# Kernel tuning notes

Measured on AMD Instinct MI355X. Metric: run time of the kernel, lower is better.

## Reference

```python
import jax, jax.numpy as jnp
import numpy as np

NUM_BINS = 256
SCALAR = 1.0


def _per_batch_hist(img):
    # img: [B, C, H, W] in [0,1]. torch.histc(img[i]*255, bins=256, min=0, max=255)
    # bin width = 255/256; value v maps to bin floor(v * 256/255), last edge -> bin 255.
    B = img.shape[0]
    x = img.reshape(B, -1) * 255.0
    idx = jnp.clip(jnp.floor(x * (NUM_BINS / 255.0)), 0, NUM_BINS - 1).astype(jnp.int32)
    # offset bin ids per batch item so one segment_sum builds all histograms
    seg = idx + (jnp.arange(B, dtype=jnp.int32)[:, None] * NUM_BINS)
    ones = jnp.ones_like(x)
    hist = jax.ops.segment_sum(ones.ravel(), seg.ravel(), num_segments=B * NUM_BINS)
    hist = hist.reshape(B, NUM_BINS)
    hist = hist / jnp.sum(hist, axis=1, keepdims=True)
    return hist.T  # [NUM_BINS, B] matching torch.stack(hist, dim=1)


def setup_inputs() -> dict:
    key = jax.random.key(0)
    k1, k2 = jax.random.split(key)
    im1 = jax.random.uniform(k1, (16, 3, 512, 512), dtype=jnp.float32)
    im2 = jax.random.uniform(k2, (16, 3, 512, 512), dtype=jnp.float32)
    return {"im1": im1, "im2": im2}


def reference(im1, im2):
    h1 = _per_batch_hist(im1)  # [256, B]
    h2 = _per_batch_hist(im2)
    c1 = jnp.cumsum(h1, axis=0)
    c2 = jnp.cumsum(h2, axis=0)
    emd = jnp.sum(jnp.abs(c1 - c2), axis=0)  # L1 over bin dim -> [B]
    total = jnp.sum(emd) / h2.shape[0] * SCALAR / 3.0
    return total
```

## Files before the change

### kernel.cpp

```cpp
#include <hip/hip_runtime.h>

#define NUM_BINS 256
#define PER_HIST 786432
#define BATCH 16
#define NHIST 32
#define CHUNKS 64
#define THREADS 256
#define ELEMS_PER_BLOCK (PER_HIST / CHUNKS)
#define VEC_PER_BLOCK (ELEMS_PER_BLOCK / 4)
#define ITERS (VEC_PER_BLOCK / THREADS)

typedef float floatx4 __attribute__((ext_vector_type(4)));

__global__ void zero_ws_kernel(unsigned int* __restrict__ ws) {
    ws[blockIdx.x * blockDim.x + threadIdx.x] = 0u;
}

__global__ __launch_bounds__(THREADS) void hist_kernel(const float* __restrict__ im1,
                                                       const float* __restrict__ im2,
                                                       unsigned int* __restrict__ hist) {
    __shared__ unsigned int lh[4][NUM_BINS];
    const int t = threadIdx.x;
    const int w = t >> 6;

    #pragma unroll
    for (int i = 0; i < 4; ++i) lh[i][t] = 0u;
    __syncthreads();

    const int hid = blockIdx.y;
    const float* src = (hid < BATCH) ? im1 : im2;
    const int batch = hid & (BATCH - 1);
    const floatx4* p = (const floatx4*)(src + (size_t)batch * PER_HIST
                                            + (size_t)blockIdx.x * ELEMS_PER_BLOCK);

    const float c255 = 255.0f;
    const float scale = (float)NUM_BINS / 255.0f;

    #pragma unroll
    for (int i = 0; i < ITERS; ++i) {
        floatx4 v = __builtin_nontemporal_load(&p[i * THREADS + t]);
        #pragma unroll
        for (int j = 0; j < 4; ++j) {
            float x = v[j] * c255;
            float tt = x * scale;
            int idx = (int)tt;
            idx = idx > (NUM_BINS - 1) ? (NUM_BINS - 1) : idx;
            idx = idx < 0 ? 0 : idx;
            atomicAdd(&lh[w][idx], 1u);
        }
    }
    __syncthreads();

    unsigned int sum = lh[0][t] + lh[1][t] + lh[2][t] + lh[3][t];
    atomicAdd(&hist[hid * NUM_BINS + t], sum);
}

__global__ __launch_bounds__(1024) void emd_kernel(const unsigned int* __restrict__ hist,
                                                   float* __restrict__ out) {
    __shared__ int batch_emd[BATCH];
    const int t = threadIdx.x;
    const int w = t >> 6;
    const int lane = t & 63;

    const uint4* h1 = (const uint4*)(hist + w * NUM_BINS);
    const uint4* h2 = (const uint4*)(hist + (BATCH + w) * NUM_BINS);
    uint4 a = h1[lane];
    uint4 b = h2[lane];

    int d0 = (int)a.x - (int)b.x;
    int d1 = (int)a.y - (int)b.y;
    int d2 = (int)a.z - (int)b.z;
    int d3 = (int)a.w - (int)b.w;

    int p0 = d0;
    int p1 = p0 + d1;
    int p2 = p1 + d2;
    int p3 = p2 + d3;

    int s = p3;
    #pragma unroll
    for (int off = 1; off < 64; off <<= 1) {
        int v = __shfl_up(s, off, 64);
        if (lane >= off) s += v;
    }
    int excl = s - p3;

    int c0 = excl + p0, c1 = excl + p1, c2 = excl + p2, c3 = excl + p3;
    int aa = (c0 < 0 ? -c0 : c0) + (c1 < 0 ? -c1 : c1)
           + (c2 < 0 ? -c2 : c2) + (c3 < 0 ? -c3 : c3);

    #pragma unroll
    for (int off = 32; off > 0; off >>= 1) aa += __shfl_xor(aa, off, 64);

    if (lane == 0) batch_emd[w] = aa;
    __syncthreads();

    if (t == 0) {
        long long acc = 0;
        #pragma unroll
        for (int i = 0; i < BATCH; ++i) acc += (long long)batch_emd[i];
        double total = (double)acc / (double)PER_HIST / (double)NUM_BINS / 3.0;
        out[0] = (float)total;
    }
}

extern "C" void kernel_launch(void* const* d_in, const int* in_sizes, int n_in,
                              void* d_out, int out_size, void* d_ws, size_t ws_size,
                              hipStream_t stream) {
    const float* im1 = (const float*)d_in[0];
    const float* im2 = (const float*)d_in[1];
    unsigned int* hist = (unsigned int*)d_ws;
    float* out = (float*)d_out;

    zero_ws_kernel<<<NHIST * NUM_BINS / THREADS, THREADS, 0, stream>>>(hist);

    dim3 grid(CHUNKS, NHIST);
    hist_kernel<<<grid, THREADS, 0, stream>>>(im1, im2, hist);

    emd_kernel<<<1, 1024, 0, stream>>>(hist, out);
}
```

Baseline: 121.2 us.

## Replace global atomic histogram merge with per-block partials and parallel reduction

Each histogram block now writes its 256-bin partial to its own slot in the workspace instead of atomically adding into a shared global histogram, which removes the zeroing kernel. A new 16-block kernel sums the 64 chunk partials per batch and computes the EMD per batch with a block-wide scan. A tiny finalize kernel sums the per-batch results. This trades the global atomics and zero pass for an extra kernel launch and about 2 MB of partial reads.

```diff
diff --git a/kernel.cpp b/kernel.cpp
--- a/kernel.cpp
+++ b/kernel.cpp
@@ -12,13 +12,11 @@
 
 typedef float floatx4 __attribute__((ext_vector_type(4)));
 
-__global__ void zero_ws_kernel(unsigned int* __restrict__ ws) {
-    ws[blockIdx.x * blockDim.x + threadIdx.x] = 0u;
-}
+#define PART_WORDS (NHIST * CHUNKS * NUM_BINS)
 
 __global__ __launch_bounds__(THREADS) void hist_kernel(const float* __restrict__ im1,
                                                        const float* __restrict__ im2,
-                                                       unsigned int* __restrict__ hist) {
+                                                       unsigned int* __restrict__ part) {
     __shared__ unsigned int lh[4][NUM_BINS];
     const int t = threadIdx.x;
     const int w = t >> 6;
@@ -52,54 +50,62 @@
     __syncthreads();
 
     unsigned int sum = lh[0][t] + lh[1][t] + lh[2][t] + lh[3][t];
-    atomicAdd(&hist[hid * NUM_BINS + t], sum);
+    part[((size_t)hid * CHUNKS + blockIdx.x) * NUM_BINS + t] = sum;
 }
 
-__global__ __launch_bounds__(1024) void emd_kernel(const unsigned int* __restrict__ hist,
-                                                   float* __restrict__ out) {
-    __shared__ int batch_emd[BATCH];
+__global__ __launch_bounds__(THREADS) void emd_batch_kernel(const unsigned int* __restrict__ part,
+                                                            long long* __restrict__ bemd) {
+    __shared__ int wave_sums[4];
     const int t = threadIdx.x;
     const int w = t >> 6;
     const int lane = t & 63;
+    const int b = blockIdx.x;
 
-    const uint4* h1 = (const uint4*)(hist + w * NUM_BINS);
-    const uint4* h2 = (const uint4*)(hist + (BATCH + w) * NUM_BINS);
-    uint4 a = h1[lane];
-    uint4 b = h2[lane];
+    const unsigned int* p1 = part + (size_t)b * CHUNKS * NUM_BINS;
+    const unsigned int* p2 = part + (size_t)(BATCH + b) * CHUNKS * NUM_BINS;
 
-    int d0 = (int)a.x - (int)b.x;
-    int d1 = (int)a.y - (int)b.y;
-    int d2 = (int)a.z - (int)b.z;
-    int d3 = (int)a.w - (int)b.w;
+    int s1 = 0, s2 = 0;
+    #pragma unroll 8
+    for (int c = 0; c < CHUNKS; ++c) {
+        s1 += (int)p1[c * NUM_BINS + t];
+        s2 += (int)p2[c * NUM_BINS + t];
+    }
+    int d = s1 - s2;
 
-    int p0 = d0;
-    int p1 = p0 + d1;
-    int p2 = p1 + d2;
-    int p3 = p2 + d3;
-
-    int s = p3;
+    int s = d;
     #pragma unroll
     for (int off = 1; off < 64; off <<= 1) {
         int v = __shfl_up(s, off, 64);
         if (lane >= off) s += v;
     }
-    int excl = s - p3;
+    if (lane == 63) wave_sums[w] = s;
+    __syncthreads();
 
-    int c0 = excl + p0, c1 = excl + p1, c2 = excl + p2, c3 = excl + p3;
-    int aa = (c0 < 0 ? -c0 : c0) + (c1 < 0 ? -c1 : c1)
-           + (c2 < 0 ? -c2 : c2) + (c3 < 0 ? -c3 : c3);
+    int wave_off = 0;
+    #pragma unroll
+    for (int i = 0; i < 4; ++i) wave_off += (i < w) ? wave_sums[i] : 0;
+    int cdf = wave_off + s;
+    int a = cdf < 0 ? -cdf : cdf;
 
     #pragma unroll
-    for (int off = 32; off > 0; off >>= 1) aa += __shfl_xor(aa, off, 64);
+    for (int off = 32; off > 0; off >>= 1) a += __shfl_xor(a, off, 64);
+    __syncthreads();
+    if (lane == 0) wave_sums[w] = a;
+    __syncthreads();
+    if (t == 0) {
+        long long tot = (long long)wave_sums[0] + wave_sums[1] + wave_sums[2] + wave_sums[3];
+        bemd[b] = tot;
+    }
+}
 
-    if (lane == 0) batch_emd[w] = aa;
-    __syncthreads();
-
-    if (t == 0) {
-        long long acc = 0;
-        #pragma unroll
-        for (int i = 0; i < BATCH; ++i) acc += (long long)batch_emd[i];
-        double total = (double)acc / (double)PER_HIST / (double)NUM_BINS / 3.0;
+__global__ __launch_bounds__(64) void finalize_kernel(const long long* __restrict__ bemd,
+                                                      float* __restrict__ out) {
+    const int lane = threadIdx.x;
+    long long v = (lane < BATCH) ? bemd[lane] : 0LL;
+    #pragma unroll
+    for (int off = 32; off > 0; off >>= 1) v += __shfl_xor(v, off, 64);
+    if (lane == 0) {
+        double total = (double)v / (double)PER_HIST / (double)NUM_BINS / 3.0;
         out[0] = (float)total;
     }
 }
@@ -109,13 +115,14 @@
                               hipStream_t stream) {
     const float* im1 = (const float*)d_in[0];
     const float* im2 = (const float*)d_in[1];
-    unsigned int* hist = (unsigned int*)d_ws;
+    unsigned int* part = (unsigned int*)d_ws;
+    long long* bemd = (long long*)((char*)d_ws + PART_WORDS * sizeof(unsigned int));
     float* out = (float*)d_out;
 
-    zero_ws_kernel<<<NHIST * NUM_BINS / THREADS, THREADS, 0, stream>>>(hist);
+    dim3 grid(CHUNKS, NHIST);
+    hist_kernel<<<grid, THREADS, 0, stream>>>(im1, im2, part);
 
-    dim3 grid(CHUNKS, NHIST);
-    hist_kernel<<<grid, THREADS, 0, stream>>>(im1, im2, hist);
+    emd_batch_kernel<<<BATCH, THREADS, 0, stream>>>(part, bemd);
 
-    emd_kernel<<<1, 1024, 0, stream>>>(hist, out);
+    finalize_kernel<<<1, 64, 0, stream>>>(bemd, out);
 }
```

Measured after the change: 125.0 us. +3.1%, slower.
